# Performance work log

Hardware: AMD Instinct MI355X
Metric: run time of the kernel (lower is better)

## Reference

```python
import jax, jax.numpy as jnp
import numpy as np

N = 8192        # batch_size (number of nodes)
E = 262144      # number of edges
VD = 256        # vertex_dim
ED = 256        # edge_dim
HD = 512        # hid_dim
DAMPING = 0.45
EPS = 1e-5      # BatchNorm1d default eps


def setup_inputs() -> dict:
    key = jax.random.key(0)
    ks = jax.random.split(key, 8)
    def lin_w(k, out_d, in_d):
        # kaiming-uniform-ish scale, fp32
        lim = 1.0 / np.sqrt(in_d)
        return jax.random.uniform(k, (out_d, in_d), jnp.float32, -lim, lim)
    return {
        "x": jax.random.normal(ks[0], (N, VD), jnp.float32),
        "edge_weight": jax.random.normal(ks[1], (E, ED), jnp.float32),
        "edge_index": jax.random.randint(ks[2], (2, E), 0, N),
        "W0": lin_w(ks[3], HD, VD), "b0": jnp.zeros((HD,), jnp.float32),
        "Ww0": lin_w(ks[4], HD, ED), "bw0": jnp.zeros((HD,), jnp.float32),
        "W1": lin_w(ks[5], VD, HD), "b1": jnp.zeros((VD,), jnp.float32),
        "Ww1": lin_w(ks[6], ED, HD), "bw1": jnp.zeros((ED,), jnp.float32),
        "gamma": jnp.ones((HD,), jnp.float32),
        "beta": jnp.zeros((HD,), jnp.float32),
    }


def reference(x, edge_weight, edge_index, W0, b0, Ww0, bw0, W1, b1, Ww1, bw1, gamma, beta):
    out = x @ W0.T + b0                       # [N, HD]
    w = edge_weight @ Ww0.T + bw0             # [E, HD]
    src = edge_index[0]                       # [E]
    # The per-node python loop in the original is an exact segment reduction:
    # out[i] += damping * sum of w over edges with src==i (pre-update w),
    # then w[e] += damping * scalar_sum(out_new[src[e]])  (t.sum over hid dim).
    out = out + DAMPING * jax.ops.segment_sum(w, src, num_segments=N)
    node_scalar = jnp.sum(out, axis=1)        # [N] scalar per node
    w = w + DAMPING * node_scalar[src][:, None]
    # cauchy selector: cosine similarity minus identity, row-softmax mix
    nrm = jnp.sqrt(jnp.sum(out * out, axis=1, keepdims=True))   # [N,1]
    sim = (out @ out.T) / (nrm @ nrm.T) - jnp.eye(N, dtype=out.dtype)
    out = jax.nn.softmax(sim, axis=1) @ out   # [N, HD]
    # BatchNorm1d in training mode (batch stats, biased variance)
    mean = jnp.mean(w, axis=0)
    var = jnp.mean((w - mean) ** 2, axis=0)
    w = (w - mean) * jax.lax.rsqrt(var + EPS) * gamma + beta
    return out @ W1.T + b1, w @ Ww1.T + bw1
```

## Files before the change

kernel.cpp:

```cpp
#include <hip/hip_runtime.h>

typedef unsigned short u16;
typedef __attribute__((ext_vector_type(8))) short bh8;
typedef __attribute__((ext_vector_type(4))) float f4v;

#define NN 8192
#define EE 262144
#define VDIM 256
#define EDIM 256
#define HDIM 512
#define DAMP 0.45f

__device__ __forceinline__ float b2f(u16 u){ unsigned int x = ((unsigned int)u)<<16; return __builtin_bit_cast(float, x); }
__device__ __forceinline__ u16 f2b(float f){ unsigned int x = __builtin_bit_cast(unsigned int, f); x = (x + 0x7fffu + ((x>>16)&1u)) >> 16; return (u16)x; }

__device__ __forceinline__ void gload16(const void* g, void* l){
  __builtin_amdgcn_global_load_lds((const __attribute__((address_space(1))) void*)g,
                                   (__attribute__((address_space(3))) void*)l, 16, 0, 0);
}

__global__ __launch_bounds__(256) void k_hist(const int* __restrict__ src, int* __restrict__ deg){
  int e = blockIdx.x*256 + threadIdx.x;
  if (e < EE) atomicAdd(&deg[src[e]], 1);
}

__global__ __launch_bounds__(1024) void k_scan(const int* __restrict__ deg, int* __restrict__ ofs, int* __restrict__ cur){
  __shared__ int lds[1024];
  int t = threadIdx.x;
  int v[8], pre[8]; int s = 0;
  #pragma unroll
  for (int j=0;j<8;++j){ v[j] = deg[t*8+j]; }
  #pragma unroll
  for (int j=0;j<8;++j){ pre[j] = s; s += v[j]; }
  lds[t] = s; __syncthreads();
  int run = s;
  for (int off=1; off<1024; off<<=1){
    int x = (t>=off) ? lds[t-off] : 0;
    __syncthreads();
    lds[t] += x;
    __syncthreads();
  }
  int excl = lds[t] - run;
  #pragma unroll
  for (int j=0;j<8;++j){ int o = excl + pre[j]; ofs[t*8+j] = o; cur[t*8+j] = o; }
  if (t == 1023) ofs[NN] = excl + run;
}

__global__ __launch_bounds__(256) void k_permute(const int* __restrict__ src, int* __restrict__ cur,
                                                 int* __restrict__ pos, int* __restrict__ elist){
  int e = blockIdx.x*256 + threadIdx.x;
  if (e < EE){ int p = atomicAdd(&cur[src[e]], 1); pos[e] = p; elist[p] = e; }
}

__global__ __launch_bounds__(256) void k_cvtW(const float* __restrict__ in, u16* __restrict__ out, int n8){
  int i = blockIdx.x*256 + threadIdx.x;
  if (i < n8){
    const f4v* p = (const f4v*)(in + (size_t)i*8);
    f4v f0 = p[0], f1 = p[1];
    bh8 v;
    #pragma unroll
    for (int j=0;j<4;++j){ v[j]=(short)f2b(f0[j]); v[j+4]=(short)f2b(f1[j]); }
    ((bh8*)out)[i] = v;
  }
}

template<int A_BF16, int B_BF16, int EPI>
__global__ __launch_bounds__(256)
void k_gemm(const void* __restrict__ Aptr, const void* __restrict__ Bptr,
            int M, int N, int K, const float* __restrict__ bias,
            void* __restrict__ Cptr,
            const float* __restrict__ invnA, float* __restrict__ lsum)
{
  __shared__ u16 As[128*32];
  __shared__ u16 Bs[128*32];
  const int t = threadIdx.x;
  const int m0 = blockIdx.y*128, n0 = blockIdx.x*128;
  const int wid = t>>6, lane = t&63, l15 = lane&15, grp = lane>>4;
  const int wm = (wid>>1)*64, wn = (wid&1)*64;
  const int srow = t>>1, shalf = t&1;
  const int rlane = lane>>2, clane = lane&3;

  f4v acc[4][4];
  #pragma unroll
  for (int i=0;i<4;++i)
    #pragma unroll
    for (int j=0;j<4;++j) acc[i][j] = (f4v)0.0f;

  for (int kt=0; kt<K; kt+=32){
    __syncthreads();
    if (A_BF16){
      const u16* g0 = (const u16*)Aptr + (size_t)(m0 + wid*32 + rlane)*K + kt + clane*8;
      gload16(g0,                 &As[wid*1024]);
      gload16(g0 + (size_t)16*K,  &As[wid*1024 + 512]);
    } else {
      u16* dst = &As[srow*32 + shalf*16];
      const float* ap = (const float*)Aptr + (size_t)(m0+srow)*K + kt + shalf*16;
      const f4v* ap4 = (const f4v*)ap;
      f4v f0 = ap4[0], f1 = ap4[1], f2 = ap4[2], f3 = ap4[3];
      bh8 v0, v1;
      #pragma unroll
      for (int j=0;j<4;++j){ v0[j]=(short)f2b(f0[j]); v0[j+4]=(short)f2b(f1[j]); v1[j]=(short)f2b(f2[j]); v1[j+4]=(short)f2b(f3[j]); }
      ((bh8*)dst)[0] = v0; ((bh8*)dst)[1] = v1;
    }
    if (B_BF16){
      const u16* g0 = (const u16*)Bptr + (size_t)(n0 + wid*32 + rlane)*K + kt + clane*8;
      gload16(g0,                 &Bs[wid*1024]);
      gload16(g0 + (size_t)16*K,  &Bs[wid*1024 + 512]);
    } else {
      u16* dst = &Bs[srow*32 + shalf*16];
      const float* bp = (const float*)Bptr + (size_t)(n0+srow)*K + kt + shalf*16;
      const f4v* bp4 = (const f4v*)bp;
      f4v f0 = bp4[0], f1 = bp4[1], f2 = bp4[2], f3 = bp4[3];
      bh8 v0, v1;
      #pragma unroll
      for (int j=0;j<4;++j){ v0[j]=(short)f2b(f0[j]); v0[j+4]=(short)f2b(f1[j]); v1[j]=(short)f2b(f2[j]); v1[j+4]=(short)f2b(f3[j]); }
      ((bh8*)dst)[0] = v0; ((bh8*)dst)[1] = v1;
    }
    __syncthreads();
    bh8 af[4], bfv[4];
    #pragma unroll
    for (int f=0; f<4; ++f) af[f]  = *(const bh8*)&As[(wm + f*16 + l15)*32 + grp*8];
    #pragma unroll
    for (int f=0; f<4; ++f) bfv[f] = *(const bh8*)&Bs[(wn + f*16 + l15)*32 + grp*8];
    #pragma unroll
    for (int fi=0; fi<4; ++fi)
      #pragma unroll
      for (int fj=0; fj<4; ++fj)
        acc[fi][fj] = __builtin_amdgcn_mfma_f32_16x16x32_bf16(af[fi], bfv[fj], acc[fi][fj], 0, 0, 0);
  }

  if (EPI == 3){
    float ic[4];
    #pragma unroll
    for (int fj=0; fj<4; ++fj) ic[fj] = invnA[n0 + wn + fj*16 + l15];
    #pragma unroll
    for (int fi=0; fi<4; ++fi){
      #pragma unroll
      for (int r=0;r<4;++r){
        int rowg = m0 + wm + fi*16 + grp*4 + r;
        float iq = invnA[rowg];
        float rs = 0.f;
        #pragma unroll
        for (int fj=0; fj<4; ++fj){
          int c = n0 + wn + fj*16 + l15;
          float s = acc[fi][fj][r]*iq*ic[fj];
          float p = (rowg == c) ? 1.0f : __expf(s);
          ((u16*)Cptr)[(size_t)rowg*N + c] = f2b(p);
          rs += p;
        }
        rs += __shfl_xor(rs,1); rs += __shfl_xor(rs,2); rs += __shfl_xor(rs,4); rs += __shfl_xor(rs,8);
        if (l15 == 0) atomicAdd(&lsum[rowg], rs);
      }
    }
    return;
  }

  float ilv[4][4];
  if (EPI == 4){
    #pragma unroll
    for (int fi=0; fi<4; ++fi)
      #pragma unroll
      for (int r=0;r<4;++r)
        ilv[fi][r] = 1.0f / lsum[m0 + wm + fi*16 + grp*4 + r];
  }
  #pragma unroll
  for (int fj=0; fj<4; ++fj){
    int c = n0 + wn + fj*16 + l15;
    float bv = (EPI == 0 && bias) ? bias[c] : 0.f;
    #pragma unroll
    for (int fi=0; fi<4; ++fi){
      #pragma unroll
      for (int r=0;r<4;++r){
        size_t rowg = (size_t)(m0 + wm + fi*16 + grp*4 + r);
        float v = acc[fi][fj][r];
        if (EPI == 0)      ((float*)Cptr)[rowg*N + c] = v + bv;
        else               ((u16*)Cptr)[rowg*N + c]  = f2b(v * ilv[fi][r]);
      }
    }
  }
}

template<int A_BF16, int BN, int EPI>
__global__ __launch_bounds__(512, 2)
void k_gemmw2(const void* __restrict__ Aptr, const u16* __restrict__ Bptr,
              int K, const float* __restrict__ bias, void* __restrict__ Cptr,
              const int* __restrict__ mapArr, const int* __restrict__ srcIdx,
              const float* __restrict__ nsArr, const float* __restrict__ rowterm,
              const float* __restrict__ constterm)
{
  constexpr int NF = BN/64;
  __shared__ u16 As[128*32];
  __shared__ u16 Bs[BN*32];
  const int t = threadIdx.x;
  const int tile = ((int)blockIdx.x & 7)*((int)gridDim.x>>3) + ((int)blockIdx.x>>3);
  const int m0 = tile*128;
  const int wid = t>>6, lane = t&63, l15 = lane&15, grp = lane>>4;
  const int wm = (wid>>2)*64;
  const int wn = (wid&3)*(BN/4);

  f4v acc[4][NF];
  #pragma unroll
  for (int i=0;i<4;++i)
    #pragma unroll
    for (int j=0;j<NF;++j) acc[i][j] = (f4v)0.0f;

  for (int kt=0; kt<K; kt+=32){
    __syncthreads();
    if (A_BF16){
      const u16* g0 = (const u16*)Aptr + (size_t)(m0 + wid*16 + (lane>>2))*K + kt + (lane&3)*8;
      gload16(g0, &As[wid*512]);
    } else {
      const float* ap = (const float*)Aptr + (size_t)(m0 + (t>>2))*K + kt + (t&3)*8;
      const f4v* ap4 = (const f4v*)ap;
      f4v f0 = ap4[0], f1 = ap4[1];
      bh8 v;
      #pragma unroll
      for (int j=0;j<4;++j){ v[j]=(short)f2b(f0[j]); v[j+4]=(short)f2b(f1[j]); }
      *(bh8*)&As[(t>>2)*32 + (t&3)*8] = v;
    }
    #pragma unroll
    for (int j=0;j<BN/128;++j){
      const u16* g0 = Bptr + (size_t)(j*128 + wid*16 + (lane>>2))*K + kt + (lane&3)*8;
      gload16(g0, &Bs[wid*512 + j*4096]);
    }
    __syncthreads();
    bh8 af[4], bfv[NF];
    #pragma unroll
    for (int f=0; f<4; ++f)  af[f]  = *(const bh8*)&As[(wm + f*16 + l15)*32 + grp*8];
    #pragma unroll
    for (int f=0; f<NF; ++f) bfv[f] = *(const bh8*)&Bs[(wn + f*16 + l15)*32 + grp*8];
    #pragma unroll
    for (int fi=0; fi<4; ++fi)
      #pragma unroll
      for (int fj=0; fj<NF; ++fj)
        acc[fi][fj] = __builtin_amdgcn_mfma_f32_16x16x32_bf16(af[fi], bfv[fj], acc[fi][fj], 0, 0, 0);
  }

  int prow[4][4];
  float cvals[4][4];
  #pragma unroll
  for (int fi=0; fi<4; ++fi)
    #pragma unroll
    for (int r=0;r<4;++r){
      int slot = m0 + wm + fi*16 + grp*4 + r;
      int mp = mapArr[slot];
      prow[fi][r] = mp;
      if (EPI == 2) cvals[fi][r] = DAMP * nsArr[srcIdx[mp]];
    }
  #pragma unroll
  for (int fj=0; fj<NF; ++fj){
    int c = wn + fj*16 + l15;
    float bv = 0.f, rt = 0.f, ct = 0.f;
    if (EPI == 2){ rt = rowterm[c]; ct = constterm[c]; }
    else bv = bias[c];
    #pragma unroll
    for (int fi=0; fi<4; ++fi){
      #pragma unroll
      for (int r=0;r<4;++r){
        size_t rowg = (size_t)prow[fi][r];
        if (EPI == 5) ((u16*)Cptr)[rowg*BN + c]  = f2b(acc[fi][fj][r] + bv);
        else          ((float*)Cptr)[rowg*BN + c] = acc[fi][fj][r] + cvals[fi][r]*rt + ct;
      }
    }
  }
}

__global__ __launch_bounds__(512)
void k_segsumB(const u16* __restrict__ w0, const int* __restrict__ ofs,
               float* __restrict__ S, float* __restrict__ sqpart)
{
  __shared__ u16 lds[16*512];
  const int t = threadIdx.x, w = t>>6, lane = t&63;
  const int base = blockIdx.x*128;

  int lo = 0, hi = NN-1;
  while (lo < hi){ int mid = (lo+hi+1)>>1; if (ofs[mid] <= base) lo = mid; else hi = mid-1; }
  int ni = lo;
  int nend = ofs[ni+1];

  float acc = 0.f, sqv = 0.f;
  bool first = true;

  for (int chunk = 0; chunk < 8; ++chunk){
    __syncthreads();
    {
      const u16* r0 = w0 + (size_t)(base + chunk*16 + w)*512 + lane*8;
      gload16(r0,                  &lds[w*512]);
      gload16(r0 + (size_t)8*512,  &lds[(w+8)*512]);
    }
    __syncthreads();
    #pragma unroll
    for (int r = 0; r < 16; ++r){
      int row = base + chunk*16 + r;
      float v = b2f(lds[r*512 + t]);
      acc += v; sqv += v*v;
      if (row + 1 == nend){
        if (first){ atomicAdd(&S[(size_t)ni*512 + t], acc); first = false; }
        else        S[(size_t)ni*512 + t] = acc;
        acc = 0.f; ++ni;
        while (ni < NN-1 && ofs[ni+1] == row+1) ++ni;
        nend = ofs[ni+1];
      }
    }
  }
  if (base + 128 < nend) atomicAdd(&S[(size_t)ni*512 + t], acc);
  sqpart[(size_t)blockIdx.x*512 + t] = sqv;
}

__global__ __launch_bounds__(512)
void k_sqred(const float* __restrict__ sqpart, float* __restrict__ colsumsq){
  int t = threadIdx.x;
  float s = 0.f;
  for (int b = 0; b < 32; ++b)
    s += sqpart[(size_t)(blockIdx.x*32 + b)*512 + t];
  atomicAdd(&colsumsq[t], s);
}

__global__ __launch_bounds__(256)
void k_nodefin2(const float* __restrict__ S, const float* __restrict__ out0,
                float* __restrict__ nsA, float* __restrict__ invn, u16* __restrict__ ob)
{
  const int t = threadIdx.x, wid = t>>6, lane = t&63;
  const int node = blockIdx.x*4 + wid;
  const f4v* s4 = (const f4v*)(S + (size_t)node*512 + lane*8);
  f4v sA = s4[0], sB = s4[1];
  const f4v* o4 = (const f4v*)(out0 + (size_t)node*512 + lane*8);
  f4v qA = o4[0], qB = o4[1];
  float o[8];
  #pragma unroll
  for (int j=0;j<4;++j){ o[j] = qA[j] + DAMP*sA[j]; o[j+4] = qB[j] + DAMP*sB[j]; }
  float nsp = 0.f, qp = 0.f;
  #pragma unroll
  for (int j=0;j<8;++j){ nsp += o[j]; qp += o[j]*o[j]; }
  #pragma unroll
  for (int m=1; m<64; m<<=1){ nsp += __shfl_xor(nsp, m); qp += __shfl_xor(qp, m); }
  if (lane == 0){ nsA[node] = nsp; invn[node] = rsqrtf(qp); }
  bh8 ub;
  #pragma unroll
  for (int j=0;j<8;++j) ub[j] = (short)f2b(o[j]);
  *(bh8*)(ob + (size_t)node*512 + lane*8) = ub;
}

__global__ __launch_bounds__(512)
void k_colred(const float* __restrict__ S, const float* __restrict__ nsA,
              const int* __restrict__ ofs,
              float* __restrict__ colsum0, float* __restrict__ cross,
              float* __restrict__ sumc, float* __restrict__ sumc2)
{
  __shared__ float red1[128], red2[128];
  const int t = threadIdx.x;
  const int n0 = blockIdx.x*128;
  float cs = 0.f, cr = 0.f;
  for (int i = 0; i < 128; ++i){
    int node = n0 + i;
    float s = S[(size_t)node*512 + t];
    cs += s; cr += nsA[node]*s;
  }
  atomicAdd(&colsum0[t], cs);
  atomicAdd(&cross[t],   DAMP*cr);
  if (t < 128){
    int node = n0 + t;
    float nsv = nsA[node];
    float degf = (float)(ofs[node+1] - ofs[node]);
    red1[t] = degf*nsv;
    red2[t] = degf*nsv*nsv;
  }
  __syncthreads();
  if (t == 0){
    float s1 = 0.f, s2 = 0.f;
    #pragma unroll 8
    for (int i = 0; i < 128; ++i){ s1 += red1[i]; s2 += red2[i]; }
    atomicAdd(sumc,  DAMP*s1);
    atomicAdd(sumc2, DAMP*DAMP*s2);
  }
}

__global__ __launch_bounds__(256)
void k_transpose(const u16* __restrict__ in, u16* __restrict__ out){
  __shared__ u16 tile[64][65];
  int r0 = blockIdx.x*64, c0 = blockIdx.y*64;
  int t = threadIdx.x;
  int rr = t>>2, cc = (t&3)*16;
  const u16* ip = in + (size_t)(r0+rr)*512 + c0 + cc;
  #pragma unroll
  for (int j=0;j<16;++j) tile[rr][cc+j] = ip[j];
  __syncthreads();
  int cr = t>>2, rb = (t&3)*16;
  u16* op = out + (size_t)(c0+cr)*8192 + r0 + rb;
  #pragma unroll
  for (int j=0;j<16;++j) op[j] = tile[rb+j][cr];
}

__global__ __launch_bounds__(512)
void k_bnfinal(const float* __restrict__ colsum0, const float* __restrict__ colsumsq,
               const float* __restrict__ cross, const float* __restrict__ sumc,
               const float* __restrict__ sumc2, const float* __restrict__ gamma,
               const float* __restrict__ beta, float* __restrict__ alphaA, float* __restrict__ bbA)
{
  int j = threadIdx.x;
  const float invE = 1.0f / (float)EE;
  float mean = (colsum0[j] + sumc[0]) * invE;
  float ex2  = (colsumsq[j] + 2.f*cross[j] + sumc2[0]) * invE;
  float var  = ex2 - mean*mean;
  float is   = rsqrtf(var + 1e-5f);
  float a    = gamma[j]*is;
  alphaA[j]  = a;
  bbA[j]     = beta[j] - mean*a;
}

__global__ __launch_bounds__(512)
void k_wprime(const float* __restrict__ Ww1, const float* __restrict__ alphaA,
              const float* __restrict__ bbA, const float* __restrict__ bw1,
              u16* __restrict__ Ww1pb, float* __restrict__ rowterm, float* __restrict__ constt)
{
  __shared__ float red[512];
  int k = blockIdx.x, j = threadIdx.x;
  float wv = Ww1[(size_t)k*512 + j];
  float a  = alphaA[j];
  Ww1pb[(size_t)k*512 + j] = f2b(wv*a);
  red[j] = wv*a; __syncthreads();
  for (int off=256; off>0; off>>=1){ if (j<off) red[j] += red[j+off]; __syncthreads(); }
  if (j == 0) rowterm[k] = red[0];
  __syncthreads();
  red[j] = wv*bbA[j]; __syncthreads();
  for (int off=256; off>0; off>>=1){ if (j<off) red[j] += red[j+off]; __syncthreads(); }
  if (j == 0) constt[k] = red[0] + bw1[k];
}

extern "C" void kernel_launch(void* const* d_in, const int* in_sizes, int n_in,
                              void* d_out, int out_size, void* d_ws, size_t ws_size,
                              hipStream_t stream)
{
  const float* x    = (const float*)d_in[0];
  const float* ew   = (const float*)d_in[1];
  const int*   ei   = (const int*)  d_in[2];
  const float* W0   = (const float*)d_in[3];
  const float* b0   = (const float*)d_in[4];
  const float* Ww0  = (const float*)d_in[5];
  const float* bw0  = (const float*)d_in[6];
  const float* W1   = (const float*)d_in[7];
  const float* b1   = (const float*)d_in[8];
  const float* Ww1  = (const float*)d_in[9];
  const float* bw1  = (const float*)d_in[10];
  const float* gamma= (const float*)d_in[11];
  const float* beta = (const float*)d_in[12];
  const int* src = ei;

  char* ws = (char*)d_ws;
  u16*   w0    = (u16*)  (ws + 0ULL);
  float* out0  = (float*)(ws + 268435456ULL);
  u16*   ob    = (u16*)  (ws + 285212672ULL);
  u16*   obT   = (u16*)  (ws + 293601280ULL);
  u16*   onew  = (u16*)  (ws + 301989888ULL);
  float* nsA   = (float*)(ws + 310378496ULL);
  float* invn  = (float*)(ws + 310411264ULL);
  int*   deg   = (int*)  (ws + 310444032ULL);
  int*   ofs   = (int*)  (ws + 310476800ULL);
  int*   cur   = (int*)  (ws + 310509824ULL);
  int*   elist = (int*)  (ws + 310542592ULL);
  float* stats = (float*)(ws + 311591168ULL);
  float* cross    = stats;
  float* colsum0  = stats + 512;
  float* colsumsq = stats + 1024;
  float* sumc     = stats + 1536;
  float* sumc2    = stats + 1537;
  float* lsum   = (float*)(ws + 311607552ULL);
  u16*   Ww1pb  = (u16*)  (ws + 311640320ULL);
  float* rowterm= (float*)(ws + 312164608ULL);
  float* constt = (float*)(ws + 312165632ULL);
  float* alphaA = (float*)(ws + 312166656ULL);
  float* bbA    = (float*)(ws + 312168704ULL);
  u16*   Ww0b   = (u16*)  (ws + 312170752ULL);
  int*   pos   = (int*)onew;

  float* out1 = (float*)d_out;
  float* out2 = out1 + (size_t)NN*VDIM;
  u16*   Pbuf = (u16*)out2;
  float* S      = (float*)((char*)out2 + 251658240ULL);
  float* sqpart = (float*)((char*)out2 + 247463936ULL);

  hipMemsetAsync(deg, 0, NN*sizeof(int), stream);
  hipMemsetAsync(stats, 0, 16384, stream);
  hipMemsetAsync(lsum, 0, NN*sizeof(float), stream);
  hipMemsetAsync(S, 0, (size_t)NN*512*sizeof(float), stream);

  k_hist   <<<EE/256, 256, 0, stream>>>(src, deg);
  k_scan   <<<1, 1024, 0, stream>>>(deg, ofs, cur);
  k_permute<<<EE/256, 256, 0, stream>>>(src, cur, pos, elist);
  k_cvtW   <<<64, 256, 0, stream>>>(Ww0, Ww0b, HDIM*EDIM/8);

  k_gemmw2<0,512,5><<<2048, 512, 0, stream>>>(ew, Ww0b, EDIM, bw0, w0,
                                              pos, nullptr, nullptr, nullptr, nullptr);
  k_gemm<0,0,0><<<dim3(4,64), 256, 0, stream>>>(x, W0, NN, HDIM, VDIM, b0, out0, nullptr, nullptr);

  k_segsumB<<<2048, 512, 0, stream>>>(w0, ofs, S, sqpart);
  k_sqred  <<<64, 512, 0, stream>>>(sqpart, colsumsq);
  k_nodefin2<<<NN/4, 256, 0, stream>>>(S, out0, nsA, invn, ob);
  k_colred <<<64, 512, 0, stream>>>(S, nsA, ofs, colsum0, cross, sumc, sumc2);

  k_transpose<<<dim3(128,8), 256, 0, stream>>>(ob, obT);
  k_bnfinal<<<1, 512, 0, stream>>>(colsum0, colsumsq, cross, sumc, sumc2, gamma, beta, alphaA, bbA);
  k_wprime<<<256, 512, 0, stream>>>(Ww1, alphaA, bbA, bw1, Ww1pb, rowterm, constt);

  k_gemm<1,1,3><<<dim3(64,64), 256, 0, stream>>>(ob, ob, NN, NN, HDIM, nullptr, Pbuf, invn, lsum);
  k_gemm<1,1,4><<<dim3(4,64), 256, 0, stream>>>(Pbuf, obT, NN, HDIM, NN, nullptr, onew, nullptr, lsum);

  k_gemmw2<1,256,2><<<2048, 512, 0, stream>>>(w0, Ww1pb, HDIM, nullptr, out2,
                                              elist, src, nsA, rowterm, constt);
  k_gemm<1,0,0><<<dim3(2,64), 256, 0, stream>>>(onew, W1, NN, VDIM, HDIM, b1, out1, nullptr, nullptr);
}
```

Before: 924.0 us.

## Shrink edge-GEMM M-tile, prefetch A into registers, and replace lsum global atomics

```diff
diff --git a/kernel.cpp b/kernel.cpp
--- a/kernel.cpp
+++ b/kernel.cpp
@@ -2,6 +2,7 @@
 
 typedef unsigned short u16;
 typedef __attribute__((ext_vector_type(8))) short bh8;
+typedef __attribute__((ext_vector_type(4))) short bh4;
 typedef __attribute__((ext_vector_type(4))) float f4v;
 
 #define NN 8192
@@ -73,12 +74,15 @@
 {
   __shared__ u16 As[128*32];
   __shared__ u16 Bs[128*32];
+  __shared__ float lrow[128];
   const int t = threadIdx.x;
   const int m0 = blockIdx.y*128, n0 = blockIdx.x*128;
   const int wid = t>>6, lane = t&63, l15 = lane&15, grp = lane>>4;
   const int wm = (wid>>1)*64, wn = (wid&1)*64;
   const int srow = t>>1, shalf = t&1;
   const int rlane = lane>>2, clane = lane&3;
+
+  if (EPI == 3 && t < 128) lrow[t] = 0.f;
 
   f4v acc[4][4];
   #pragma unroll
@@ -149,9 +153,11 @@
           rs += p;
         }
         rs += __shfl_xor(rs,1); rs += __shfl_xor(rs,2); rs += __shfl_xor(rs,4); rs += __shfl_xor(rs,8);
-        if (l15 == 0) atomicAdd(&lsum[rowg], rs);
-      }
-    }
+        if (l15 == 0) atomicAdd(&lrow[wm + fi*16 + grp*4 + r], rs);
+      }
+    }
+    __syncthreads();
+    if (t < 128) lsum[(size_t)blockIdx.x*NN + m0 + t] = lrow[t];
     return;
   }
 
@@ -180,92 +186,118 @@
   }
 }
 
+__global__ __launch_bounds__(256)
+void k_lred(const float* __restrict__ lpart, float* __restrict__ lsum){
+  int i = blockIdx.x*256 + threadIdx.x;
+  float s = 0.f;
+  #pragma unroll 8
+  for (int b = 0; b < 64; ++b) s += lpart[(size_t)b*NN + i];
+  lsum[i] = s;
+}
+
 template<int A_BF16, int BN, int EPI>
-__global__ __launch_bounds__(512, 2)
-void k_gemmw2(const void* __restrict__ Aptr, const u16* __restrict__ Bptr,
+__global__ __launch_bounds__(512, 4)
+void k_gemmw3(const void* __restrict__ Aptr, const u16* __restrict__ Bptr,
               int K, const float* __restrict__ bias, void* __restrict__ Cptr,
               const int* __restrict__ mapArr, const int* __restrict__ srcIdx,
               const float* __restrict__ nsArr, const float* __restrict__ rowterm,
               const float* __restrict__ constterm)
 {
-  constexpr int NF = BN/64;
-  __shared__ u16 As[128*32];
+  constexpr int CG = BN/64;
+  constexpr int MF = (CG==8)?4:2;
+  __shared__ u16 As[64*32];
   __shared__ u16 Bs[BN*32];
   const int t = threadIdx.x;
   const int tile = ((int)blockIdx.x & 7)*((int)gridDim.x>>3) + ((int)blockIdx.x>>3);
-  const int m0 = tile*128;
+  const int m0 = tile*64;
   const int wid = t>>6, lane = t&63, l15 = lane&15, grp = lane>>4;
-  const int wm = (wid>>2)*64;
-  const int wn = (wid&3)*(BN/4);
-
-  f4v acc[4][NF];
-  #pragma unroll
-  for (int i=0;i<4;++i)
-    #pragma unroll
-    for (int j=0;j<NF;++j) acc[i][j] = (f4v)0.0f;
+  const int wn = (wid & (CG-1))*64;
+  const int wm = (wid / CG)*32;
+
+  f4v acc[MF][4];
+  #pragma unroll
+  for (int i=0;i<MF;++i)
+    #pragma unroll
+    for (int j=0;j<4;++j) acc[i][j] = (f4v)0.0f;
+
+  if (A_BF16){
+    if (wid < 4){
+      const u16* g0 = (const u16*)Aptr + (size_t)(m0 + wid*16 + (lane>>2))*K + (lane&3)*8;
+      gload16(g0, &As[wid*512]);
+    }
+  } else {
+    const float* ap = (const float*)Aptr + (size_t)(m0 + (t>>3))*K + (t&7)*4;
+    f4v f0 = *(const f4v*)ap;
+    bh4 v;
+    #pragma unroll
+    for (int j=0;j<4;++j) v[j]=(short)f2b(f0[j]);
+    *(bh4*)&As[(t>>3)*32 + (t&7)*4] = v;
+  }
+  #pragma unroll
+  for (int j=0;j<BN/128;++j){
+    const u16* g0 = Bptr + (size_t)(j*128 + wid*16 + (lane>>2))*K + (lane&3)*8;
+    gload16(g0, &Bs[wid*512 + j*4096]);
+  }
+  __syncthreads();
 
   for (int kt=0; kt<K; kt+=32){
-    __syncthreads();
-    if (A_BF16){
-      const u16* g0 = (const u16*)Aptr + (size_t)(m0 + wid*16 + (lane>>2))*K + kt + (lane&3)*8;
-      gload16(g0, &As[wid*512]);
-    } else {
-      const float* ap = (const float*)Aptr + (size_t)(m0 + (t>>2))*K + kt + (t&3)*8;
-      const f4v* ap4 = (const f4v*)ap;
-      f4v f0 = ap4[0], f1 = ap4[1];
-      bh8 v;
-      #pragma unroll
-      for (int j=0;j<4;++j){ v[j]=(short)f2b(f0[j]); v[j+4]=(short)f2b(f1[j]); }
-      *(bh8*)&As[(t>>2)*32 + (t&3)*8] = v;
-    }
-    #pragma unroll
-    for (int j=0;j<BN/128;++j){
-      const u16* g0 = Bptr + (size_t)(j*128 + wid*16 + (lane>>2))*K + kt + (lane&3)*8;
-      gload16(g0, &Bs[wid*512 + j*4096]);
-    }
-    __syncthreads();
-    bh8 af[4], bfv[NF];
-    #pragma unroll
-    for (int f=0; f<4; ++f)  af[f]  = *(const bh8*)&As[(wm + f*16 + l15)*32 + grp*8];
-    #pragma unroll
-    for (int f=0; f<NF; ++f) bfv[f] = *(const bh8*)&Bs[(wn + f*16 + l15)*32 + grp*8];
-    #pragma unroll
-    for (int fi=0; fi<4; ++fi)
-      #pragma unroll
-      for (int fj=0; fj<NF; ++fj)
+    const bool more = (kt+32 < K);
+    f4v pf; bh8 pb;
+    if (more){
+      if (A_BF16){
+        if (t < 256)
+          pb = *(const bh8*)((const u16*)Aptr + (size_t)(m0 + (t>>2))*K + kt+32 + (t&3)*8);
+      } else {
+        pf = *(const f4v*)((const float*)Aptr + (size_t)(m0 + (t>>3))*K + kt+32 + (t&7)*4);
+      }
+    }
+    bh8 af[MF], bfv[4];
+    #pragma unroll
+    for (int f=0; f<MF; ++f) af[f]  = *(const bh8*)&As[(wm + f*16 + l15)*32 + grp*8];
+    #pragma unroll
+    for (int f=0; f<4; ++f)  bfv[f] = *(const bh8*)&Bs[(wn + f*16 + l15)*32 + grp*8];
+    #pragma unroll
+    for (int fi=0; fi<MF; ++fi)
+      #pragma unroll
+      for (int fj=0; fj<4; ++fj)
         acc[fi][fj] = __builtin_amdgcn_mfma_f32_16x16x32_bf16(af[fi], bfv[fj], acc[fi][fj], 0, 0, 0);
-  }
-
-  int prow[4][4];
-  float cvals[4][4];
-  #pragma unroll
-  for (int fi=0; fi<4; ++fi)
+    __syncthreads();
+    if (more){
+      if (A_BF16){
+        if (t < 256) *(bh8*)&As[(t>>2)*32 + (t&3)*8] = pb;
+      } else {
+        bh4 v;
+        #pragma unroll
+        for (int j=0;j<4;++j) v[j]=(short)f2b(pf[j]);
+        *(bh4*)&As[(t>>3)*32 + (t&7)*4] = v;
+      }
+      #pragma unroll
+      for (int j=0;j<BN/128;++j){
+        const u16* g0 = Bptr + (size_t)(j*128 + wid*16 + (lane>>2))*K + kt+32 + (lane&3)*8;
+        gload16(g0, &Bs[wid*512 + j*4096]);
+      }
+    }
+    __syncthreads();
+  }
+
+  #pragma unroll
+  for (int fi=0; fi<MF; ++fi){
     #pragma unroll
     for (int r=0;r<4;++r){
       int slot = m0 + wm + fi*16 + grp*4 + r;
       int mp = mapArr[slot];
-      prow[fi][r] = mp;
-      if (EPI == 2) cvals[fi][r] = DAMP * nsArr[srcIdx[mp]];
-    }
-  #pragma unroll
-  for (int fj=0; fj<NF; ++fj){
-    int c = wn + fj*16 + l15;
-    float bv = 0.f, rt = 0.f, ct = 0.f;
-    if (EPI == 2){ rt = rowterm[c]; ct = constterm[c]; }
-    else bv = bias[c];
-    #pragma unroll
-    for (int fi=0; fi<4; ++fi){
-      #pragma unroll
-      for (int r=0;r<4;++r){
-        size_t rowg = (size_t)prow[fi][r];
-        if (EPI == 5) ((u16*)Cptr)[rowg*BN + c]  = f2b(acc[fi][fj][r] + bv);
-        else          ((float*)Cptr)[rowg*BN + c] = acc[fi][fj][r] + cvals[fi][r]*rt + ct;
-      }
-    }
-  }
-}
-
-__global__ __launch_bounds__(512)
+      float cv = (EPI == 2) ? DAMP * nsArr[srcIdx[mp]] : 0.f;
+      #pragma unroll
+      for (int fj=0; fj<4; ++fj){
+        int c = wn + fj*16 + l15;
+        if (EPI == 5) ((u16*)Cptr)[(size_t)mp*BN + c]  = f2b(acc[fi][fj][r] + bias[c]);
+        else          ((float*)Cptr)[(size_t)mp*BN + c] = acc[fi][fj][r] + cv*rowterm[c] + constterm[c];
+      }
+    }
+  }
+}
+
+__global__ __launch_bounds__(512, 8)
 void k_segsumB(const u16* __restrict__ w0, const int* __restrict__ ofs,
                float* __restrict__ S, float* __restrict__ sqpart)
 {
@@ -476,12 +508,12 @@
   float* out1 = (float*)d_out;
   float* out2 = out1 + (size_t)NN*VDIM;
   u16*   Pbuf = (u16*)out2;
+  float* lpart  = (float*)((char*)out2 + 167772160ULL);
+  float* sqpart = (float*)((char*)out2 + 247463936ULL);
   float* S      = (float*)((char*)out2 + 251658240ULL);
-  float* sqpart = (float*)((char*)out2 + 247463936ULL);
 
   hipMemsetAsync(deg, 0, NN*sizeof(int), stream);
   hipMemsetAsync(stats, 0, 16384, stream);
-  hipMemsetAsync(lsum, 0, NN*sizeof(float), stream);
   hipMemsetAsync(S, 0, (size_t)NN*512*sizeof(float), stream);
 
   k_hist   <<<EE/256, 256, 0, stream>>>(src, deg);
@@ -489,7 +521,7 @@
   k_permute<<<EE/256, 256, 0, stream>>>(src, cur, pos, elist);
   k_cvtW   <<<64, 256, 0, stream>>>(Ww0, Ww0b, HDIM*EDIM/8);
 
-  k_gemmw2<0,512,5><<<2048, 512, 0, stream>>>(ew, Ww0b, EDIM, bw0, w0,
+  k_gemmw3<0,512,5><<<4096, 512, 0, stream>>>(ew, Ww0b, EDIM, bw0, w0,
                                               pos, nullptr, nullptr, nullptr, nullptr);
   k_gemm<0,0,0><<<dim3(4,64), 256, 0, stream>>>(x, W0, NN, HDIM, VDIM, b0, out0, nullptr, nullptr);
 
@@ -502,10 +534,11 @@
   k_bnfinal<<<1, 512, 0, stream>>>(colsum0, colsumsq, cross, sumc, sumc2, gamma, beta, alphaA, bbA);
   k_wprime<<<256, 512, 0, stream>>>(Ww1, alphaA, bbA, bw1, Ww1pb, rowterm, constt);
 
-  k_gemm<1,1,3><<<dim3(64,64), 256, 0, stream>>>(ob, ob, NN, NN, HDIM, nullptr, Pbuf, invn, lsum);
+  k_gemm<1,1,3><<<dim3(64,64), 256, 0, stream>>>(ob, ob, NN, NN, HDIM, nullptr, Pbuf, invn, lpart);
+  k_lred<<<NN/256, 256, 0, stream>>>(lpart, lsum);
   k_gemm<1,1,4><<<dim3(4,64), 256, 0, stream>>>(Pbuf, obT, NN, HDIM, NN, nullptr, onew, nullptr, lsum);
 
-  k_gemmw2<1,256,2><<<2048, 512, 0, stream>>>(w0, Ww1pb, HDIM, nullptr, out2,
+  k_gemmw3<1,256,2><<<4096, 512, 0, stream>>>(w0, Ww1pb, HDIM, nullptr, out2,
                                               elist, src, nsA, rowterm, constt);
   k_gemm<1,0,0><<<dim3(2,64), 256, 0, stream>>>(onew, W1, NN, VDIM, HDIM, b1, out1, nullptr, nullptr);
 }
```

After: 839.4 us. 9.2% less time.
